# Kernel tuning notes

Hardware: AMD Instinct MI355X
Metric: run time of the kernel (lower is better)

## Reference

```python
import jax, jax.numpy as jnp
import numpy as np

T, B, F_, H, D, C = 16, 1024, 512, 128, 8, 100  # trees, batch, feat, hidden, depth, classes
L = 2 ** (D + 1)  # n_leaf = 512


def _routing_tables():
    # Static per-leaf routing: node index and branch side at each depth.
    # Derived from compute_mu's gather indices:
    #   node(d, l) = 2^d - 1 + l // 2^(D+1-d);  side(d, l) = (l // 2^(D-d)) % 2
    l = np.arange(L)
    node = np.stack([(2 ** d - 1) + l // (2 ** (D + 1 - d)) for d in range(D + 1)])  # [D+1, L]
    side = np.stack([(l // (2 ** (D - d))) % 2 for d in range(D + 1)])               # [D+1, L]
    return jnp.asarray(node, dtype=jnp.int32), jnp.asarray(side.astype(np.bool_))


def setup_inputs() -> dict:
    key = jax.random.key(0)
    ks = jax.random.split(key, 4)
    return {
        "feat": jax.random.normal(ks[0], (B, F_), jnp.float32),
        "W1": jax.random.normal(ks[1], (T, F_, H), jnp.float32) * 0.05,
        "b1": jnp.zeros((T, H), jnp.float32),
        "W2": jax.random.normal(ks[2], (T, H, L), jnp.float32) * 0.05,
        "b2": jnp.zeros((T, L), jnp.float32),
        "pi": jax.random.uniform(ks[3], (T, L, C), jnp.float32, -2.0, 2.0),
    }


def reference(feat, W1, b1, W2, b2, pi):
    node, side = _routing_tables()
    # Per-tree MLP head (dropout is identity in eval mode).
    h = jax.nn.relu(jnp.einsum('bf,tfh->tbh', feat, W1) + b1[:, None, :])        # [T,B,H]
    p = jax.nn.sigmoid(jnp.einsum('tbh,thl->tbl', h, W2) + b2[:, None, :])       # [T,B,L]
    # compute_mu: product of routing probs along each root->leaf path.
    sel = p[:, :, node]                          # [T,B,D+1,L] gather (static indices)
    route = jnp.where(side, 1.0 - sel, sel)      # left -> p, right -> 1-p
    mu = jnp.prod(route, axis=2)                 # [T,B,L]
    # compute_py_x: mean over leaves then mean over trees of mu @ softmax(pi).
    leaf_p = jax.nn.softmax(pi, axis=-1)         # [T,L,C]
    py_x = jnp.einsum('tbl,tlc->bc', mu, leaf_p) / (L * T)  # [B,C]
    return jnp.log(py_x)
```

## Files before the change

### kernel.cpp

```cpp
#include <hip/hip_runtime.h>
#include <hip/hip_bf16.h>
#include <math.h>

#define T_ 16
#define B_ 1024
#define F_ 512
#define H_ 128
#define D_ 8
#define C_ 100
#define L_ 512
#define CP_ 112

typedef __attribute__((ext_vector_type(8))) short bf16x8_t;
typedef __attribute__((ext_vector_type(4))) float f32x4_t;

__device__ inline ushort f2bf(float x) {
  __hip_bfloat16 b = __float2bfloat16(x);
  return *(ushort*)&b;
}
__device__ inline float bf2f(ushort u) {
  union { unsigned int i; float f; } v;
  v.i = ((unsigned int)u) << 16;
  return v.f;
}

__device__ inline void bar_raw() {
  asm volatile("" ::: "memory");
  __builtin_amdgcn_s_barrier();
  asm volatile("" ::: "memory");
}
__device__ inline void bar_publish_lds() {
  asm volatile("s_waitcnt lgkmcnt(0)" ::: "memory");
  __builtin_amdgcn_s_barrier();
  asm volatile("" ::: "memory");
}

__global__ __launch_bounds__(256) void k_prep(
    const float* __restrict__ W1, const float* __restrict__ W2,
    const float* __restrict__ pi, ushort* __restrict__ W1T,
    ushort* __restrict__ W2T, ushort* __restrict__ lpT) {
  __shared__ ushort ubuf[112 * 48];
  float (*tile)[33] = (float(*)[33])ubuf;
  ushort (*tileT)[48] = (ushort(*)[48])ubuf;
  const int bid = blockIdx.x, tid = threadIdx.x;

  if (bid < 2048) {
    const float* X; ushort* XT; int K, N, kb, nb, s;
    if (bid < 1024) {
      int r = bid;         kb = r & 15; nb = (r >> 4) & 3;  s = r >> 6;
      X = W1; XT = W1T; K = F_; N = H_;
    } else {
      int r = bid - 1024;  kb = r & 3;  nb = (r >> 2) & 15; s = r >> 6;
      X = W2; XT = W2T; K = H_; N = L_;
    }
    const int k0 = kb * 32, n0 = nb * 32;
    const int c = tid & 31, r0 = tid >> 5;
    const float* Xs = X + (size_t)s * K * N;
    ushort* XTs = XT + (size_t)s * N * K;
#pragma unroll
    for (int j = 0; j < 4; ++j)
      tile[r0 + 8 * j][c] = Xs[(size_t)(k0 + r0 + 8 * j) * N + n0 + c];
    __syncthreads();
#pragma unroll
    for (int j = 0; j < 4; ++j)
      XTs[(size_t)(n0 + r0 + 8 * j) * K + k0 + c] = f2bf(tile[c][r0 + 8 * j]);
    return;
  }
  {
    int bid2 = bid - 2048;
    int t = bid2 >> 4, l0 = (bid2 & 15) << 5;
    int lane = tid & 63;
#pragma unroll
    for (int p = 0; p < 8; ++p) {
      int rl = p * 4 + (tid >> 6);
      const float* x = pi + (size_t)(t * L_ + l0 + rl) * C_;
      float v0 = (lane < C_) ? x[lane] : -1e30f;
      float v1 = (lane + 64 < C_) ? x[lane + 64] : -1e30f;
      float m = fmaxf(v0, v1);
#pragma unroll
      for (int off = 32; off; off >>= 1) m = fmaxf(m, __shfl_xor(m, off, 64));
      float e0 = __expf(v0 - m);
      float e1 = (lane + 64 < C_) ? __expf(v1 - m) : 0.0f;
      float sm = e0 + e1;
#pragma unroll
      for (int off = 32; off; off >>= 1) sm += __shfl_xor(sm, off, 64);
      float inv = 1.0f / sm;
      if (lane < C_) tileT[lane][rl] = f2bf(e0 * inv);
      int c2 = lane + 64;
      if (c2 < CP_) tileT[c2][rl] = f2bf(c2 < C_ ? e1 * inv : 0.0f);
    }
    __syncthreads();
    ushort* dst = lpT + (size_t)t * CP_ * L_ + l0;
    for (int idx = tid; idx < 448; idx += 256) {
      int c = idx >> 2, ch = (idx & 3) * 8;
      *(bf16x8_t*)(dst + (size_t)c * L_ + ch) = *(const bf16x8_t*)&tileT[c][ch];
    }
  }
}

__global__ __launch_bounds__(512, 4) void k12_mfma(
    const float* __restrict__ feat, const ushort* __restrict__ W1T,
    const float* __restrict__ b1, const ushort* __restrict__ W2T,
    const float* __restrict__ b2, const ushort* __restrict__ lpT,
    float* __restrict__ acc_out, unsigned int* __restrict__ cnt,
    float* __restrict__ out) {
  __shared__ ushort smem[38400];
  ushort (*h_s)[136] = (ushort(*)[136])smem;
  ushort (*a_s0)[72] = (ushort(*)[72])(smem + 4352);
  ushort (*a_s1)[72] = (ushort(*)[72])(smem + 4352 + 2304);
  ushort (*b_s0)[72] = (ushort(*)[72])(smem + 8960);
  ushort (*b_s1)[72] = (ushort(*)[72])(smem + 8960 + 9216);
  ushort (*w_s0)[136] = (ushort(*)[136])(smem + 4352);
  ushort (*w_s1)[136] = (ushort(*)[136])(smem + 4352 + 8704);
  ushort (*p_s)[520] = (ushort(*)[520])(smem + 21760);
  __shared__ unsigned int last_flag;

  const int bid = blockIdx.x;
  const int t = bid & 15, b0 = (bid >> 4) * 32;
  const int tid = threadIdx.x;
  const int w = tid >> 6, lane = tid & 63, quad = lane >> 4, n = lane & 15;

  {
    const bool doA = tid < 256;
    const int srow = tid >> 3, scol = (tid & 7) * 8;
    const float*  fp32p = feat + (size_t)(b0 + srow) * F_ + scol;
    const ushort* w1p   = W1T + ((size_t)t * H_ + srow) * F_ + scol;

    float4 ra[2][2];
    bf16x8_t rb[2][2];

    if (doA) { ra[0][0] = *(const float4*)(fp32p);
               ra[0][1] = *(const float4*)(fp32p + 4); }
#pragma unroll
    for (int i = 0; i < 2; ++i)
      rb[0][i] = *(const bf16x8_t*)(w1p + (size_t)i * 64 * F_);
    if (doA) {
      bf16x8_t o;
      o[0] = (short)f2bf(ra[0][0].x); o[1] = (short)f2bf(ra[0][0].y);
      o[2] = (short)f2bf(ra[0][0].z); o[3] = (short)f2bf(ra[0][0].w);
      o[4] = (short)f2bf(ra[0][1].x); o[5] = (short)f2bf(ra[0][1].y);
      o[6] = (short)f2bf(ra[0][1].z); o[7] = (short)f2bf(ra[0][1].w);
      *(bf16x8_t*)&a_s0[srow][scol] = o;
    }
#pragma unroll
    for (int i = 0; i < 2; ++i)
      *(bf16x8_t*)&b_s0[i * 64 + srow][scol] = rb[0][i];
    bar_publish_lds();
    if (doA) { ra[1][0] = *(const float4*)(fp32p + 64);
               ra[1][1] = *(const float4*)(fp32p + 68); }
#pragma unroll
    for (int i = 0; i < 2; ++i)
      rb[1][i] = *(const bf16x8_t*)(w1p + (size_t)i * 64 * F_ + 64);
    if (doA) { ra[0][0] = *(const float4*)(fp32p + 128);
               ra[0][1] = *(const float4*)(fp32p + 132); }
#pragma unroll
    for (int i = 0; i < 2; ++i)
      rb[0][i] = *(const bf16x8_t*)(w1p + (size_t)i * 64 * F_ + 128);

    f32x4_t acc[2];
    acc[0] = (f32x4_t){0.f, 0.f, 0.f, 0.f};
    acc[1] = (f32x4_t){0.f, 0.f, 0.f, 0.f};
#pragma unroll
    for (int kc = 0; kc < 8; ++kc) {
      ushort (*ar)[72] = (kc & 1) ? a_s1 : a_s0;
      ushort (*br)[72] = (kc & 1) ? b_s1 : b_s0;
#pragma unroll
      for (int ks2 = 0; ks2 < 2; ++ks2) {
        const int ko = ks2 * 32 + quad * 8;
        bf16x8_t af0 = *(const bf16x8_t*)&ar[n][ko];
        bf16x8_t af1 = *(const bf16x8_t*)&ar[16 + n][ko];
        bf16x8_t bfr = *(const bf16x8_t*)&br[w * 16 + n][ko];
        acc[0] = __builtin_amdgcn_mfma_f32_16x16x32_bf16(af0, bfr, acc[0],
                                                         0, 0, 0);
        acc[1] = __builtin_amdgcn_mfma_f32_16x16x32_bf16(af1, bfr, acc[1],
                                                         0, 0, 0);
      }
      if (kc < 7) {
        const int p = (kc + 1) & 1;
        ushort (*aw)[72] = p ? a_s1 : a_s0;
        ushort (*bw)[72] = p ? b_s1 : b_s0;
        if (doA) {
          bf16x8_t o;
          o[0] = (short)f2bf(ra[p][0].x); o[1] = (short)f2bf(ra[p][0].y);
          o[2] = (short)f2bf(ra[p][0].z); o[3] = (short)f2bf(ra[p][0].w);
          o[4] = (short)f2bf(ra[p][1].x); o[5] = (short)f2bf(ra[p][1].y);
          o[6] = (short)f2bf(ra[p][1].z); o[7] = (short)f2bf(ra[p][1].w);
          *(bf16x8_t*)&aw[srow][scol] = o;
        }
#pragma unroll
        for (int i = 0; i < 2; ++i)
          *(bf16x8_t*)&bw[i * 64 + srow][scol] = rb[p][i];
        bar_publish_lds();
        if (kc < 6) {
          if (doA) { ra[p][0] = *(const float4*)(fp32p + (kc + 3) * 64);
                     ra[p][1] = *(const float4*)(fp32p + (kc + 3) * 64 + 4); }
#pragma unroll
          for (int i = 0; i < 2; ++i)
            rb[p][i] = *(const bf16x8_t*)(w1p + (size_t)i * 64 * F_ + (kc + 3) * 64);
        }
      }
    }
    float bias = b1[t * H_ + w * 16 + n];
#pragma unroll
    for (int mt = 0; mt < 2; ++mt)
#pragma unroll
      for (int r = 0; r < 4; ++r) {
        float v = acc[mt][r] + bias;
        h_s[mt * 16 + quad * 4 + r][w * 16 + n] = f2bf(v > 0.f ? v : 0.f);
      }
  }

  {
    const int wrow = tid >> 4, wcol = (tid & 15) * 8;
    const ushort* w2p = W2T + ((size_t)t * L_ + wrow) * H_ + wcol;
    bf16x8_t rw[2][2];
#pragma unroll
    for (int i = 0; i < 2; ++i)
      rw[0][i] = *(const bf16x8_t*)(w2p + (size_t)(i * 32) * H_);
#pragma unroll
    for (int i = 0; i < 2; ++i)
      rw[1][i] = *(const bf16x8_t*)(w2p + (size_t)(64 + i * 32) * H_);
    bar_publish_lds();

    const int mhalf = w >> 2, lhalf = w & 3;
    bf16x8_t af2[4];
#pragma unroll
    for (int ks = 0; ks < 4; ++ks)
      af2[ks] = *(const bf16x8_t*)&h_s[mhalf * 16 + n][ks * 32 + quad * 8];
#pragma unroll
    for (int i = 0; i < 2; ++i)
      *(bf16x8_t*)&w_s0[i * 32 + wrow][wcol] = rw[0][i];
    bar_publish_lds();
#pragma unroll
    for (int i = 0; i < 2; ++i)
      rw[0][i] = *(const bf16x8_t*)(w2p + (size_t)(128 + i * 32) * H_);

#pragma unroll
    for (int nc = 0; nc < 8; ++nc) {
      ushort (*wr)[136] = (nc & 1) ? w_s1 : w_s0;
      f32x4_t acc = (f32x4_t){0.f, 0.f, 0.f, 0.f};
#pragma unroll
      for (int ks = 0; ks < 4; ++ks) {
        bf16x8_t bfrag = *(const bf16x8_t*)&wr[lhalf * 16 + n][ks * 32 + quad * 8];
        acc = __builtin_amdgcn_mfma_f32_16x16x32_bf16(af2[ks], bfrag, acc,
                                                      0, 0, 0);
      }
      int l = nc * 64 + lhalf * 16 + n;
      float bias = b2[t * L_ + l];
#pragma unroll
      for (int r = 0; r < 4; ++r) {
        float x = acc[r] + bias;
        p_s[mhalf * 16 + quad * 4 + r][l] = f2bf(1.0f / (1.0f + __expf(-x)));
      }
      if (nc < 7) {
        const int p = (nc + 1) & 1;
        ushort (*ww)[136] = p ? w_s1 : w_s0;
#pragma unroll
        for (int i = 0; i < 2; ++i)
          *(bf16x8_t*)&ww[i * 32 + wrow][wcol] = rw[p][i];
        bar_publish_lds();
        if (nc < 6) {
#pragma unroll
          for (int i = 0; i < 2; ++i)
            rw[p][i] = *(const bf16x8_t*)(w2p + (size_t)((nc + 3) * 64 + i * 32) * H_);
        }
      }
    }
  }
  bar_publish_lds();

  bf16x8_t mo[2][2];
#pragma unroll
  for (int pass = 0; pass < 2; ++pass) {
    int unit = pass * 512 + tid;
    int b = unit >> 5;
    int s = unit & 31;
    float P = 1.f;
#pragma unroll
    for (int d = 0; d < 5; ++d) {
      int nd = (1 << d) - 1 + (s >> (5 - d));
      int sd = (s >> (4 - d)) & 1;
      float pv = bf2f(p_s[b][nd]);
      P *= sd ? (1.f - pv) : pv;
    }
    float p5 = bf2f(p_s[b][31 + s]);
    float q5[2] = {P * p5, P * (1.f - p5)};
    float q6[4], q7[8];
#pragma unroll
    for (int j = 0; j < 2; ++j) {
      float pv = bf2f(p_s[b][63 + 2 * s + j]);
      q6[2 * j] = q5[j] * pv;
      q6[2 * j + 1] = q5[j] * (1.f - pv);
    }
#pragma unroll
    for (int u = 0; u < 4; ++u) {
      float pv = bf2f(p_s[b][127 + 4 * s + u]);
      q7[2 * u] = q6[u] * pv;
      q7[2 * u + 1] = q6[u] * (1.f - pv);
    }
    bf16x8_t o0, o1;
#pragma unroll
    for (int v = 0; v < 8; ++v) {
      float pv = bf2f(p_s[b][255 + 8 * s + v]);
      ushort e0 = f2bf(q7[v] * pv);
      ushort e1 = f2bf(q7[v] * (1.f - pv));
      if (v < 4) { o0[2 * v] = (short)e0; o0[2 * v + 1] = (short)e1; }
      else       { o1[2 * (v - 4)] = (short)e0; o1[2 * (v - 4) + 1] = (short)e1; }
    }
    mo[pass][0] = o0;
    mo[pass][1] = o1;
  }
  bar_raw();
#pragma unroll
  for (int pass = 0; pass < 2; ++pass) {
    int unit = pass * 512 + tid;
    int b = unit >> 5;
    int s = unit & 31;
    *(bf16x8_t*)&p_s[b][s * 16]     = mo[pass][0];
    *(bf16x8_t*)&p_s[b][s * 16 + 8] = mo[pass][1];
  }
  bar_publish_lds();

  {
#pragma unroll
    for (int uu = 0; uu < 2; ++uu) {
      int u = w + uu * 8;
      if (u < 14) {
        const int mt = u & 1, nt = u >> 1;
        const ushort* arow = &p_s[mt * 16 + n][0];
        const ushort* brow = lpT + (size_t)t * CP_ * L_ +
                             ((size_t)(nt * 16 + n)) * L_ + quad * 8;
        f32x4_t acc = (f32x4_t){0.f, 0.f, 0.f, 0.f};
#pragma unroll 4
        for (int k = 0; k < L_; k += 32) {
          bf16x8_t af = *(const bf16x8_t*)(arow + k + quad * 8);
          bf16x8_t bfr = *(const bf16x8_t*)(brow + k);
          acc = __builtin_amdgcn_mfma_f32_16x16x32_bf16(af, bfr, acc, 0, 0, 0);
        }
        const int m0 = b0 + mt * 16 + quad * 4;
        const int c = nt * 16 + n;
        if (c < C_) {
#pragma unroll
          for (int r = 0; r < 4; ++r)
            atomicAdd(&acc_out[(size_t)(m0 + r) * C_ + c], acc[r]);
        }
      }
    }
  }

  __syncthreads();
  if (tid == 0) {
    __threadfence();
    unsigned int old = __hip_atomic_fetch_add(&cnt[bid >> 4], 1u,
                                              __ATOMIC_ACQ_REL,
                                              __HIP_MEMORY_SCOPE_AGENT);
    last_flag = (old == 15u) ? 1u : 0u;
  }
  __syncthreads();
  if (last_flag) {
    const float inv = 1.0f / (L_ * T_);
    for (int idx = tid; idx < 32 * C_; idx += 512) {
      size_t gi = (size_t)b0 * C_ + idx;
      float s = __hip_atomic_load(&acc_out[gi], __ATOMIC_RELAXED,
                                  __HIP_MEMORY_SCOPE_AGENT);
      out[gi] = logf(s * inv);
    }
  }
}

extern "C" void kernel_launch(void* const* d_in, const int* in_sizes, int n_in,
                              void* d_out, int out_size, void* d_ws,
                              size_t ws_size, hipStream_t stream) {
  const float* feat = (const float*)d_in[0];
  const float* W1   = (const float*)d_in[1];
  const float* b1   = (const float*)d_in[2];
  const float* W2   = (const float*)d_in[3];
  const float* b2   = (const float*)d_in[4];
  const float* pi   = (const float*)d_in[5];
  float* out = (float*)d_out;

  char* ws = (char*)d_ws;
  ushort* W1T_buf  = (ushort*)(ws);
  ushort* W2T_buf  = (ushort*)(ws + ((size_t)2 << 20));
  ushort* lpT_buf  = (ushort*)(ws + ((size_t)4 << 20));
  float*  acc_buf  = (float*)(ws + ((size_t)6 << 20));
  unsigned int* cnt_buf =
      (unsigned int*)(ws + ((size_t)6 << 20) + 409600);

  hipMemsetAsync(acc_buf, 0, 409600 + 128, stream);

  k_prep<<<2304, 256, 0, stream>>>(W1, W2, pi, W1T_buf, W2T_buf, lpT_buf);
  k12_mfma<<<512, 512, 0, stream>>>(feat, W1T_buf, b1, W2T_buf, b2,
                                    lpT_buf, acc_buf, cnt_buf, out);
}
```

Baseline: 127.2 us.

## Use per-tree partial buffers instead of atomics and widen transpose tiles

The final reduction no longer does float atomicAdd into a shared accumulator. Each tree block now writes plain stores into a per-tree partial buffer, and the last-arriving block sums the 16 partials before taking the log. This removes atomic contention and shrinks the memset to just the counters. The prep transpose now uses 64x64 tiles with float4 loads and 8-wide bf16 stores, cutting its block count and making its memory accesses wider. In exchange it uses more workspace (about 6.5 MB of partials) and adds extra reads in the finalizing blocks.

```diff
diff --git a/kernel.cpp b/kernel.cpp
--- a/kernel.cpp
+++ b/kernel.cpp
@@ -39,35 +39,46 @@
     const float* __restrict__ W1, const float* __restrict__ W2,
     const float* __restrict__ pi, ushort* __restrict__ W1T,
     ushort* __restrict__ W2T, ushort* __restrict__ lpT) {
-  __shared__ ushort ubuf[112 * 48];
-  float (*tile)[33] = (float(*)[33])ubuf;
-  ushort (*tileT)[48] = (ushort(*)[48])ubuf;
+  __shared__ float tile[64][68];
+  ushort (*tileT)[48] = (ushort(*)[48])tile;
   const int bid = blockIdx.x, tid = threadIdx.x;
 
-  if (bid < 2048) {
+  if (bid < 512) {
     const float* X; ushort* XT; int K, N, kb, nb, s;
-    if (bid < 1024) {
-      int r = bid;         kb = r & 15; nb = (r >> 4) & 3;  s = r >> 6;
+    if (bid < 256) {
+      int u = bid & 15;  kb = u & 7;  nb = (u >> 3) & 1;  s = bid >> 4;
       X = W1; XT = W1T; K = F_; N = H_;
     } else {
-      int r = bid - 1024;  kb = r & 3;  nb = (r >> 2) & 15; s = r >> 6;
+      int r = bid - 256; int u = r & 15; kb = u & 1; nb = (u >> 1) & 7; s = r >> 4;
       X = W2; XT = W2T; K = H_; N = L_;
     }
-    const int k0 = kb * 32, n0 = nb * 32;
-    const int c = tid & 31, r0 = tid >> 5;
+    const int k0 = kb * 64, n0 = nb * 64;
     const float* Xs = X + (size_t)s * K * N;
     ushort* XTs = XT + (size_t)s * N * K;
-#pragma unroll
-    for (int j = 0; j < 4; ++j)
-      tile[r0 + 8 * j][c] = Xs[(size_t)(k0 + r0 + 8 * j) * N + n0 + c];
+    {
+      const int rrow = tid >> 4, c4 = (tid & 15) * 4;
+#pragma unroll
+      for (int j = 0; j < 4; ++j) {
+        float4 v = *(const float4*)(Xs + (size_t)(k0 + j * 16 + rrow) * N + n0 + c4);
+        *(float4*)&tile[j * 16 + rrow][c4] = v;
+      }
+    }
     __syncthreads();
-#pragma unroll
-    for (int j = 0; j < 4; ++j)
-      XTs[(size_t)(n0 + r0 + 8 * j) * K + k0 + c] = f2bf(tile[c][r0 + 8 * j]);
+    {
+      const int k8 = (tid & 7) * 8;
+#pragma unroll
+      for (int pass = 0; pass < 2; ++pass) {
+        int rr = pass * 32 + (tid >> 3);
+        bf16x8_t o;
+#pragma unroll
+        for (int i = 0; i < 8; ++i) o[i] = (short)f2bf(tile[k8 + i][rr]);
+        *(bf16x8_t*)(XTs + (size_t)(n0 + rr) * K + k0 + k8) = o;
+      }
+    }
     return;
   }
   {
-    int bid2 = bid - 2048;
+    int bid2 = bid - 512;
     int t = bid2 >> 4, l0 = (bid2 & 15) << 5;
     int lane = tid & 63;
 #pragma unroll
@@ -102,7 +113,7 @@
     const float* __restrict__ feat, const ushort* __restrict__ W1T,
     const float* __restrict__ b1, const ushort* __restrict__ W2T,
     const float* __restrict__ b2, const ushort* __restrict__ lpT,
-    float* __restrict__ acc_out, unsigned int* __restrict__ cnt,
+    float* __restrict__ part, unsigned int* __restrict__ cnt,
     float* __restrict__ out) {
   __shared__ ushort smem[38400];
   ushort (*h_s)[136] = (ushort(*)[136])smem;
@@ -342,7 +353,7 @@
         if (c < C_) {
 #pragma unroll
           for (int r = 0; r < 4; ++r)
-            atomicAdd(&acc_out[(size_t)(m0 + r) * C_ + c], acc[r]);
+            part[((size_t)t * B_ + m0 + r) * C_ + c] = acc[r];
         }
       }
     }
@@ -360,10 +371,12 @@
   if (last_flag) {
     const float inv = 1.0f / (L_ * T_);
     for (int idx = tid; idx < 32 * C_; idx += 512) {
-      size_t gi = (size_t)b0 * C_ + idx;
-      float s = __hip_atomic_load(&acc_out[gi], __ATOMIC_RELAXED,
-                                  __HIP_MEMORY_SCOPE_AGENT);
-      out[gi] = logf(s * inv);
+      float s = 0.f;
+#pragma unroll
+      for (int tt = 0; tt < T_; ++tt)
+        s += __hip_atomic_load(&part[((size_t)tt * B_ + b0) * C_ + idx],
+                               __ATOMIC_RELAXED, __HIP_MEMORY_SCOPE_AGENT);
+      out[(size_t)b0 * C_ + idx] = logf(s * inv);
     }
   }
 }
@@ -383,13 +396,13 @@
   ushort* W1T_buf  = (ushort*)(ws);
   ushort* W2T_buf  = (ushort*)(ws + ((size_t)2 << 20));
   ushort* lpT_buf  = (ushort*)(ws + ((size_t)4 << 20));
-  float*  acc_buf  = (float*)(ws + ((size_t)6 << 20));
+  float*  part_buf = (float*)(ws + ((size_t)6 << 20));
   unsigned int* cnt_buf =
-      (unsigned int*)(ws + ((size_t)6 << 20) + 409600);
-
-  hipMemsetAsync(acc_buf, 0, 409600 + 128, stream);
-
-  k_prep<<<2304, 256, 0, stream>>>(W1, W2, pi, W1T_buf, W2T_buf, lpT_buf);
+      (unsigned int*)(ws + ((size_t)13 << 20));
+
+  hipMemsetAsync(cnt_buf, 0, 128, stream);
+
+  k_prep<<<768, 256, 0, stream>>>(W1, W2, pi, W1T_buf, W2T_buf, lpT_buf);
   k12_mfma<<<512, 512, 0, stream>>>(feat, W1T_buf, b1, W2T_buf, b2,
-                                    lpT_buf, acc_buf, cnt_buf, out);
-}
+                                    lpT_buf, part_buf, cnt_buf, out);
+}
```

After: 138.6 us. 1.09x slower.
